# Performance work log

Hardware: AMD Instinct MI355X
Metric: run time of the kernel (lower is better)

Reference implementation:

```python
import jax, jax.numpy as jnp
import numpy as np

N, E, G = 100000, 1600000, 64
IN, H, OUT = 128, 64, 16  # hidden/2 = 32
SLOPE = 0.01


def setup_inputs() -> dict:
    key = jax.random.key(0)
    ks = jax.random.split(key, 7)
    features = jax.random.normal(ks[0], (N, IN), dtype=jnp.float32)
    src = jax.random.randint(ks[1], (E,), 0, N)
    dst = jax.random.randint(ks[2], (E,), 0, N)
    graph_ids = jnp.sort(jax.random.randint(ks[3], (N,), 0, G))
    # kaiming-uniform-ish fan_in init, bias=False everywhere
    W1 = jax.random.uniform(ks[4], (IN, H), jnp.float32, -1.0, 1.0) * np.sqrt(3.0 / IN)
    W2 = jax.random.uniform(ks[5], (H, H // 2), jnp.float32, -1.0, 1.0) * np.sqrt(3.0 / H)
    Wc = jax.random.uniform(ks[6], (H // 2, OUT), jnp.float32, -1.0, 1.0) * np.sqrt(3.0 / (H // 2))
    return {"features": features, "src": src, "dst": dst, "graph_ids": graph_ids,
            "W1": W1, "W2": W2, "Wc": Wc}


def _graph_conv(x, W, src, dst, n):
    # DGL GraphConv, norm='both', bias=False:
    # out = D_in^{-1/2} A (D_out^{-1/2} x) W   (degrees clamped to >= 1)
    ones = jnp.ones(src.shape[0], dtype=x.dtype)
    outdeg = jnp.clip(jax.ops.segment_sum(ones, src, num_segments=n), 1.0)
    indeg = jnp.clip(jax.ops.segment_sum(ones, dst, num_segments=n), 1.0)
    h = (x * jax.lax.rsqrt(outdeg)[:, None]) @ W  # project first (in_dim > out_dim)
    m = jax.ops.segment_sum(h[src], dst, num_segments=n)  # sparse aggregation
    return m * jax.lax.rsqrt(indeg)[:, None]


def reference(features, src, dst, graph_ids, W1, W2, Wc):
    h = jax.nn.leaky_relu(_graph_conv(features, W1, src, dst, N), SLOPE)
    h = jax.nn.leaky_relu(_graph_conv(h, W2, src, dst, N), SLOPE)
    # dropout is identity at inference
    sums = jax.ops.segment_sum(h, graph_ids, num_segments=G)
    cnts = jnp.clip(jax.ops.segment_sum(jnp.ones((N,), h.dtype), graph_ids, num_segments=G), 1.0)
    mean = sums / cnts[:, None]  # dgl.mean_nodes
    return mean @ Wc  # [G, OUT]
```

## Files before the change

### kernel.cpp

```cpp
#include <hip/hip_runtime.h>

#define NN 100000
#define NE 1600000
#define NG 64
#define D_IN 128
#define D_H 64
#define D_H2 32
#define D_OUT 16
#define SLOPE 0.01f
#define REC 48

#define BSH 9
#define NBK 196
#define NCB 250
#define CHE (NE / NCB)
#define PCAP 80

typedef _Float16 half2v __attribute__((ext_vector_type(2)));
typedef _Float16 h8 __attribute__((ext_vector_type(8)));
typedef float f32x4 __attribute__((ext_vector_type(4)));

__global__ __launch_bounds__(256) void p12_scatter(const int* __restrict__ src,
                                                   const int* __restrict__ dst,
                                                   unsigned* __restrict__ pkD,
                                                   unsigned short* __restrict__ pkS,
                                                   int* __restrict__ cntD,
                                                   int* __restrict__ cntS) {
  __shared__ int cD[NBK], cS[NBK];
  int b = blockIdx.x, t = threadIdx.x;
  for (int i = t; i < NBK; i += 256) { cD[i] = 0; cS[i] = 0; }
  __syncthreads();
  const int4* s4 = (const int4*)(src + b * CHE);
  const int4* d4 = (const int4*)(dst + b * CHE);
  for (int i = t; i < CHE / 4; i += 256) {
    int4 s = s4[i], d = d4[i];
#pragma unroll
    for (int j = 0; j < 4; ++j) {
      int ss = (j == 0) ? s.x : (j == 1) ? s.y : (j == 2) ? s.z : s.w;
      int dd = (j == 0) ? d.x : (j == 1) ? d.y : (j == 2) ? d.z : d.w;
      int kd = dd >> BSH;
      int pd = atomicAdd(&cD[kd], 1);
      if (pd < PCAP) pkD[((size_t)kd * NCB + b) * PCAP + pd] =
          ((unsigned)(dd & 511) << 17) | (unsigned)ss;
      int ks = ss >> BSH;
      int ps = atomicAdd(&cS[ks], 1);
      if (ps < PCAP) pkS[((size_t)ks * NCB + b) * PCAP + ps] =
          (unsigned short)(ss & 511);
    }
  }
  __syncthreads();
  for (int i = t; i < NBK; i += 256) {
    cntD[i * NCB + b] = min(cD[i], PCAP);
    cntS[i * NCB + b] = min(cS[i], PCAP);
  }
}

__global__ __launch_bounds__(256) void p3_build(const unsigned* __restrict__ pkD,
                                                const unsigned short* __restrict__ pkS,
                                                const int* __restrict__ cntD,
                                                const int* __restrict__ cntS,
                                                int* __restrict__ adj,
                                                int* __restrict__ indeg,
                                                int* __restrict__ outdeg) {
  __shared__ int hh[512];
  int bb = blockIdx.x, t = threadIdx.x;
  for (int i = t; i < 512; i += 256) hh[i] = 0;
  __syncthreads();
  if (bb < NBK) {
    int k = bb;
    int n0 = k << BSH;
    if (t < NCB) {
      int cnt = cntD[k * NCB + t];
      const uint4* r4 = (const uint4*)(pkD + ((size_t)k * NCB + t) * PCAP);
      for (int i = 0; i * 4 < cnt; ++i) {
        uint4 v = r4[i];
#pragma unroll
        for (int j = 0; j < 4; ++j) {
          int idx = i * 4 + j;
          if (idx < cnt) {
            unsigned rec = (j == 0) ? v.x : (j == 1) ? v.y : (j == 2) ? v.z : v.w;
            int local = rec >> 17;
            int pos = atomicAdd(&hh[local], 1);
            if (pos < REC) adj[(size_t)(n0 + local) * REC + pos] = (int)(rec & 0x1FFFF);
          }
        }
      }
    }
    __syncthreads();
    int4 ph = make_int4(NN, NN, NN, NN);
    for (int i = t; i < 512; i += 256) {
      int n = n0 + i;
      if (n < NN) {
        int dg = hh[i];
        indeg[n] = dg;
        int d = min(dg, REC);
        int dr = min((d + 15) & ~15, REC);
        int j = d;
        for (; j & 3; ++j) if (j < dr) adj[(size_t)n * REC + j] = NN;
        for (; j + 4 <= dr; j += 4) *(int4*)&adj[(size_t)n * REC + j] = ph;
      }
    }
  } else {
    int k = bb - NBK;
    if (t < NCB) {
      int cnt = cntS[k * NCB + t];
      const uint4* r4 = (const uint4*)(pkS + ((size_t)k * NCB + t) * PCAP);
      for (int i = 0; i * 8 < cnt; ++i) {
        uint4 v = r4[i];
        const unsigned short* u = (const unsigned short*)&v;
#pragma unroll
        for (int j = 0; j < 8; ++j) {
          int idx = i * 8 + j;
          if (idx < cnt) atomicAdd(&hh[u[j]], 1);
        }
      }
    }
    __syncthreads();
    int n0 = k << BSH;
    for (int i = t; i < 512; i += 256) {
      int n = n0 + i;
      if (n < NN) outdeg[n] = hh[i];
    }
  }
}

__global__ __launch_bounds__(256) void k_mm1f(const float* __restrict__ X,
                                              const float* __restrict__ W,
                                              const int* __restrict__ odeg,
                                              _Float16* __restrict__ Y) {
  __shared__ _Float16 Wt[64][136];
  int t = threadIdx.x;
  if (blockIdx.x == 0 && t < 64) Y[(size_t)NN * 64 + t] = (_Float16)0.f;
  for (int i = t; i < 128 * 64; i += 256) {
    int k = i >> 6, f = i & 63;
    Wt[f][k] = (_Float16)W[i];
  }
  __syncthreads();
  int lane = t & 63, w = t >> 6;
  int m = lane & 15, q = lane >> 4;
  h8 bf[4][4];
#pragma unroll
  for (int kc = 0; kc < 4; ++kc)
#pragma unroll
    for (int nt = 0; nt < 4; ++nt)
      bf[kc][nt] = *(const h8*)&Wt[nt * 16 + m][kc * 32 + q * 8];

  const int NT = NN / 16;
  int idx = blockIdx.x * 4 + w;
  int t0 = idx * 2, t1 = t0 + 1;
  f32x4 r0[8], r1[8];
  if (t0 < NT) {
    const f32x4* X0 = (const f32x4*)(X + (size_t)(t0 * 16 + m) * 128);
#pragma unroll
    for (int kc = 0; kc < 4; ++kc) {
      r0[kc * 2 + 0] = X0[kc * 8 + q * 2 + 0];
      r0[kc * 2 + 1] = X0[kc * 8 + q * 2 + 1];
    }
  }
  if (t1 < NT) {
    const f32x4* X1 = (const f32x4*)(X + (size_t)(t1 * 16 + m) * 128);
#pragma unroll
    for (int kc = 0; kc < 4; ++kc) {
      r1[kc * 2 + 0] = X1[kc * 8 + q * 2 + 0];
      r1[kc * 2 + 1] = X1[kc * 8 + q * 2 + 1];
    }
  }
#pragma unroll
  for (int half = 0; half < 2; ++half) {
    int tile = (half == 0) ? t0 : t1;
    if (tile >= NT) continue;
    f32x4* rr = (half == 0) ? r0 : r1;
    f32x4 acc[4] = {{0,0,0,0},{0,0,0,0},{0,0,0,0},{0,0,0,0}};
#pragma unroll
    for (int kc = 0; kc < 4; ++kc) {
      f32x4 x0 = rr[kc * 2 + 0], x1 = rr[kc * 2 + 1];
      h8 a;
      a[0] = (_Float16)x0.x; a[1] = (_Float16)x0.y;
      a[2] = (_Float16)x0.z; a[3] = (_Float16)x0.w;
      a[4] = (_Float16)x1.x; a[5] = (_Float16)x1.y;
      a[6] = (_Float16)x1.z; a[7] = (_Float16)x1.w;
#pragma unroll
      for (int nt = 0; nt < 4; ++nt)
        acc[nt] = __builtin_amdgcn_mfma_f32_16x16x32_f16(a, bf[kc][nt], acc[nt], 0, 0, 0);
    }
    int n0 = tile * 16;
#pragma unroll
    for (int reg = 0; reg < 4; ++reg) {
      int nn = n0 + q * 4 + reg;
      float sc = rsqrtf((float)max(odeg[nn], 1));
#pragma unroll
      for (int nt = 0; nt < 4; ++nt)
        Y[(size_t)nn * 64 + nt * 16 + m] = (_Float16)(acc[nt][reg] * sc);
    }
  }
}

__global__ __launch_bounds__(256) void k_aggmm2(const int* __restrict__ adj,
                                                const int* __restrict__ indeg,
                                                const int* __restrict__ odeg,
                                                const h8* __restrict__ H8,
                                                const float* __restrict__ W,
                                                _Float16* __restrict__ Y) {
  __shared__ _Float16 Ht[32][72];
  __shared__ _Float16 Wt[32][72];
  int t = threadIdx.x;
  if (blockIdx.x == 0 && t < 32) Y[(size_t)NN * 32 + t] = (_Float16)0.f;
  for (int i = t; i < 64 * 32; i += 256) {
    int k = i >> 5, f = i & 31;
    Wt[f][k] = (_Float16)W[i];
  }
  int l8 = t & 7;
  int nd = t >> 3;
  int node = blockIdx.x * 32 + nd;
  int deg = indeg[node];
  int groups = (min(deg, REC) + 15) >> 4;
  const int4* c4 = (const int4*)(adj + (size_t)node * REC);
  float acc[8] = {0.f, 0.f, 0.f, 0.f, 0.f, 0.f, 0.f, 0.f};
  for (int g = 0; g < groups; ++g) {
    int4 ca = c4[g * 4 + 0], cb = c4[g * 4 + 1];
    {
      h8 v0 = H8[(size_t)ca.x * 8 + l8];
      h8 v1 = H8[(size_t)ca.y * 8 + l8];
      h8 v2 = H8[(size_t)ca.z * 8 + l8];
      h8 v3 = H8[(size_t)ca.w * 8 + l8];
      h8 v4 = H8[(size_t)cb.x * 8 + l8];
      h8 v5 = H8[(size_t)cb.y * 8 + l8];
      h8 v6 = H8[(size_t)cb.z * 8 + l8];
      h8 v7 = H8[(size_t)cb.w * 8 + l8];
#pragma unroll
      for (int j = 0; j < 8; ++j)
        acc[j] += (((float)v0[j] + (float)v1[j]) + ((float)v2[j] + (float)v3[j])) +
                  (((float)v4[j] + (float)v5[j]) + ((float)v6[j] + (float)v7[j]));
    }
    int4 cc = c4[g * 4 + 2], cd = c4[g * 4 + 3];
    {
      h8 v0 = H8[(size_t)cc.x * 8 + l8];
      h8 v1 = H8[(size_t)cc.y * 8 + l8];
      h8 v2 = H8[(size_t)cc.z * 8 + l8];
      h8 v3 = H8[(size_t)cc.w * 8 + l8];
      h8 v4 = H8[(size_t)cd.x * 8 + l8];
      h8 v5 = H8[(size_t)cd.y * 8 + l8];
      h8 v6 = H8[(size_t)cd.z * 8 + l8];
      h8 v7 = H8[(size_t)cd.w * 8 + l8];
#pragma unroll
      for (int j = 0; j < 8; ++j)
        acc[j] += (((float)v0[j] + (float)v1[j]) + ((float)v2[j] + (float)v3[j])) +
                  (((float)v4[j] + (float)v5[j]) + ((float)v6[j] + (float)v7[j]));
    }
  }
  float sc = rsqrtf((float)max(deg, 1));
  h8 hv;
#pragma unroll
  for (int j = 0; j < 8; ++j) {
    float x = acc[j] * sc;
    hv[j] = (_Float16)((x > 0.f) ? x : SLOPE * x);
  }
  *(h8*)&Ht[nd][l8 * 8] = hv;
  __syncthreads();
  int lane = t & 63, w = t >> 6;
  if (w < 2) {
    int m = lane & 15, q = lane >> 4;
    h8 bf[2][2];
#pragma unroll
    for (int kc = 0; kc < 2; ++kc)
#pragma unroll
      for (int nt = 0; nt < 2; ++nt)
        bf[kc][nt] = *(const h8*)&Wt[nt * 16 + m][kc * 32 + q * 8];
    h8 af[2];
#pragma unroll
    for (int kc = 0; kc < 2; ++kc)
      af[kc] = *(const h8*)&Ht[w * 16 + m][kc * 32 + q * 8];
    f32x4 acc2[2] = {{0, 0, 0, 0}, {0, 0, 0, 0}};
#pragma unroll
    for (int kc = 0; kc < 2; ++kc)
#pragma unroll
      for (int nt = 0; nt < 2; ++nt)
        acc2[nt] = __builtin_amdgcn_mfma_f32_16x16x32_f16(af[kc], bf[kc][nt], acc2[nt], 0, 0, 0);
#pragma unroll
    for (int reg = 0; reg < 4; ++reg) {
      int nn = blockIdx.x * 32 + w * 16 + q * 4 + reg;
      float sco = rsqrtf((float)max(odeg[nn], 1));
#pragma unroll
      for (int nt = 0; nt < 2; ++nt)
        Y[(size_t)nn * 32 + nt * 16 + m] = (_Float16)(acc2[nt][reg] * sco);
    }
  }
}

__global__ __launch_bounds__(256) void k_agg32p(const int* __restrict__ adj,
                                                const int* __restrict__ indeg,
                                                const int* __restrict__ gid,
                                                const h8* __restrict__ H8,
                                                float* __restrict__ pool) {
  __shared__ float lp[4][D_H2];
  __shared__ int gmin_s;
  int t = threadIdx.x;
  int l4 = t & 3;
  int nd = t >> 2;
  int node = blockIdx.x * 64 + nd;
  bool valid = node < NN;
  int nclamp = valid ? node : NN - 1;
  if (t == 0) gmin_s = gid[blockIdx.x * 64];
  for (int i = t; i < 4 * D_H2; i += 256) ((float*)lp)[i] = 0.f;
  int deg = valid ? indeg[nclamp] : 0;
  int groups = (min(deg, REC) + 15) >> 4;
  const int4* c4 = (const int4*)(adj + (size_t)nclamp * REC);
  float acc[8] = {0.f, 0.f, 0.f, 0.f, 0.f, 0.f, 0.f, 0.f};
  for (int g = 0; g < groups; ++g) {
    int4 ca = c4[g * 4 + 0], cb = c4[g * 4 + 1];
    {
      h8 v0 = H8[(size_t)ca.x * 4 + l4];
      h8 v1 = H8[(size_t)ca.y * 4 + l4];
      h8 v2 = H8[(size_t)ca.z * 4 + l4];
      h8 v3 = H8[(size_t)ca.w * 4 + l4];
      h8 v4 = H8[(size_t)cb.x * 4 + l4];
      h8 v5 = H8[(size_t)cb.y * 4 + l4];
      h8 v6 = H8[(size_t)cb.z * 4 + l4];
      h8 v7 = H8[(size_t)cb.w * 4 + l4];
#pragma unroll
      for (int j = 0; j < 8; ++j)
        acc[j] += (((float)v0[j] + (float)v1[j]) + ((float)v2[j] + (float)v3[j])) +
                  (((float)v4[j] + (float)v5[j]) + ((float)v6[j] + (float)v7[j]));
    }
    int4 cc = c4[g * 4 + 2], cd = c4[g * 4 + 3];
    {
      h8 v0 = H8[(size_t)cc.x * 4 + l4];
      h8 v1 = H8[(size_t)cc.y * 4 + l4];
      h8 v2 = H8[(size_t)cc.z * 4 + l4];
      h8 v3 = H8[(size_t)cc.w * 4 + l4];
      h8 v4 = H8[(size_t)cd.x * 4 + l4];
      h8 v5 = H8[(size_t)cd.y * 4 + l4];
      h8 v6 = H8[(size_t)cd.z * 4 + l4];
      h8 v7 = H8[(size_t)cd.w * 4 + l4];
#pragma unroll
      for (int j = 0; j < 8; ++j)
        acc[j] += (((float)v0[j] + (float)v1[j]) + ((float)v2[j] + (float)v3[j])) +
                  (((float)v4[j] + (float)v5[j]) + ((float)v6[j] + (float)v7[j]));
    }
  }
  __syncthreads();
  if (valid) {
    float sc = rsqrtf((float)max(deg, 1));
    int gl = min(gid[node] - gmin_s, 3);
#pragma unroll
    for (int j = 0; j < 8; ++j) {
      float x = acc[j] * sc;
      x = (x > 0.f) ? x : SLOPE * x;
      atomicAdd(&lp[gl][l4 * 8 + j], x);
    }
  }
  __syncthreads();
  if (t < 4 * D_H2) {
    float v = ((float*)lp)[t];
    if (v != 0.f) {
      int gl = t >> 5, f = t & 31;
      atomicAdd(&pool[(gmin_s + gl) * D_H2 + f], v);
    }
  }
}

__global__ __launch_bounds__(256) void k_out(const float* __restrict__ pool,
                                             const int* __restrict__ gid,
                                             const float* __restrict__ Wc,
                                             float* __restrict__ out) {
  __shared__ int bnd[NG + 1];
  __shared__ float mean[NG][D_H2];
  int t = threadIdx.x;
  if (t <= NG) {
    int target = t;
    int lo = 0, hi = NN;
    while (lo < hi) {
      int mid = (lo + hi) >> 1;
      if (gid[mid] < target) lo = mid + 1; else hi = mid;
    }
    bnd[t] = lo;
  }
  __syncthreads();
  for (int i = t; i < NG * D_H2; i += 256) {
    int g = i >> 5;
    float inv = 1.0f / (float)max(bnd[g + 1] - bnd[g], 1);
    ((float*)mean)[i] = pool[i] * inv;
  }
  __syncthreads();
  for (int i = t; i < NG * D_OUT; i += 256) {
    int g = i / D_OUT, o = i % D_OUT;
    float s = 0.f;
#pragma unroll
    for (int c = 0; c < D_H2; ++c) s += mean[g][c] * Wc[c * D_OUT + o];
    out[i] = s;
  }
}

extern "C" void kernel_launch(void* const* d_in, const int* in_sizes, int n_in,
                              void* d_out, int out_size, void* d_ws, size_t ws_size,
                              hipStream_t stream) {
  const float* X  = (const float*)d_in[0];
  const int*   src = (const int*)d_in[1];
  const int*   dst = (const int*)d_in[2];
  const int*   gid = (const int*)d_in[3];
  const float* W1 = (const float*)d_in[4];
  const float* W2 = (const float*)d_in[5];
  const float* Wc = (const float*)d_in[6];
  float* out = (float*)d_out;

  char* p = (char*)d_ws;
  auto alloc = [&](size_t bytes) {
    char* q = p;
    p += (bytes + 255) & ~(size_t)255;
    return q;
  };
  float*          pool   = (float*)alloc(NG * D_H2 * 4);
  int*            outdeg = (int*)alloc(NN * 4);
  int*            indeg  = (int*)alloc(NN * 4);
  int*            cntD   = (int*)alloc((size_t)NBK * NCB * 4);
  int*            cntS   = (int*)alloc((size_t)NBK * NCB * 4);
  unsigned*       pkD    = (unsigned*)alloc((size_t)NBK * NCB * PCAP * 4);
  unsigned short* pkS    = (unsigned short*)alloc((size_t)NBK * NCB * PCAP * 2);
  int*            adj    = (int*)alloc((size_t)NN * REC * 4);
  _Float16*       bufA   = (_Float16*)alloc((size_t)(NN + 1) * 64 * 2);
  _Float16*       bufC   = (_Float16*)alloc((size_t)(NN + 1) * 32 * 2);

  hipMemsetAsync(pool, 0, NG * D_H2 * 4, stream);

  p12_scatter<<<NCB, 256, 0, stream>>>(src, dst, pkD, pkS, cntD, cntS);
  p3_build<<<2 * NBK, 256, 0, stream>>>(pkD, pkS, cntD, cntS, adj, indeg, outdeg);

  k_mm1f<<<782, 256, 0, stream>>>(X, W1, outdeg, bufA);
  k_aggmm2<<<NN / 32, 256, 0, stream>>>(adj, indeg, outdeg, (const h8*)bufA, W2, bufC);
  k_agg32p<<<(NN + 63) / 64, 256, 0, stream>>>(adj, indeg, gid, (const h8*)bufC, pool);
  k_out<<<1, 256, 0, stream>>>(pool, gid, Wc, out);
}
```

Baseline: 219.2 us.

## Stage adjacency rows in LDS and pad neighbor lists to 8 instead of 16

The aggregation kernels now copy each block's adjacency rows and degrees into shared memory with coalesced int4 loads, then read neighbor indices from LDS. Neighbor lists are padded to a multiple of 8 rather than 16, so fewer dummy gathers of the padding node are issued. The edge-partition count doubles to 500 with a smaller per-bucket cap, and the build kernel loops over buckets to match. The costs are extra LDS use per block, an added barrier, and a higher chance of bucket overflow under the smaller cap.

```diff
diff --git a/kernel.cpp b/kernel.cpp
--- a/kernel.cpp
+++ b/kernel.cpp
@@ -12,9 +12,9 @@
 
 #define BSH 9
 #define NBK 196
-#define NCB 250
+#define NCB 500
 #define CHE (NE / NCB)
-#define PCAP 80
+#define PCAP 56
 
 typedef _Float16 half2v __attribute__((ext_vector_type(2)));
 typedef _Float16 h8 __attribute__((ext_vector_type(8)));
@@ -69,9 +69,9 @@
   if (bb < NBK) {
     int k = bb;
     int n0 = k << BSH;
-    if (t < NCB) {
-      int cnt = cntD[k * NCB + t];
-      const uint4* r4 = (const uint4*)(pkD + ((size_t)k * NCB + t) * PCAP);
+    for (int s = t; s < NCB; s += 256) {
+      int cnt = cntD[k * NCB + s];
+      const uint4* r4 = (const uint4*)(pkD + ((size_t)k * NCB + s) * PCAP);
       for (int i = 0; i * 4 < cnt; ++i) {
         uint4 v = r4[i];
 #pragma unroll
@@ -94,7 +94,7 @@
         int dg = hh[i];
         indeg[n] = dg;
         int d = min(dg, REC);
-        int dr = min((d + 15) & ~15, REC);
+        int dr = min((d + 7) & ~7, REC);
         int j = d;
         for (; j & 3; ++j) if (j < dr) adj[(size_t)n * REC + j] = NN;
         for (; j + 4 <= dr; j += 4) *(int4*)&adj[(size_t)n * REC + j] = ph;
@@ -102,9 +102,9 @@
     }
   } else {
     int k = bb - NBK;
-    if (t < NCB) {
-      int cnt = cntS[k * NCB + t];
-      const uint4* r4 = (const uint4*)(pkS + ((size_t)k * NCB + t) * PCAP);
+    for (int s = t; s < NCB; s += 256) {
+      int cnt = cntS[k * NCB + s];
+      const uint4* r4 = (const uint4*)(pkS + ((size_t)k * NCB + s) * PCAP);
       for (int i = 0; i * 8 < cnt; ++i) {
         uint4 v = r4[i];
         const unsigned short* u = (const unsigned short*)&v;
@@ -201,6 +201,8 @@
                                                 const h8* __restrict__ H8,
                                                 const float* __restrict__ W,
                                                 _Float16* __restrict__ Y) {
+  __shared__ int Adj[32][REC];
+  __shared__ int Deg[32];
   __shared__ _Float16 Ht[32][72];
   __shared__ _Float16 Wt[32][72];
   int t = threadIdx.x;
@@ -209,44 +211,34 @@
     int k = i >> 5, f = i & 31;
     Wt[f][k] = (_Float16)W[i];
   }
+  int node0 = blockIdx.x * 32;
+  {
+    const int4* gadj = (const int4*)(adj + (size_t)node0 * REC);
+    for (int i = t; i < 32 * (REC / 4); i += 256)
+      ((int4*)Adj)[i] = gadj[i];
+    if (t < 32) Deg[t] = indeg[node0 + t];
+  }
+  __syncthreads();
   int l8 = t & 7;
   int nd = t >> 3;
-  int node = blockIdx.x * 32 + nd;
-  int deg = indeg[node];
-  int groups = (min(deg, REC) + 15) >> 4;
-  const int4* c4 = (const int4*)(adj + (size_t)node * REC);
+  int deg = Deg[nd];
+  int groups = (min(deg, REC) + 7) >> 3;
   float acc[8] = {0.f, 0.f, 0.f, 0.f, 0.f, 0.f, 0.f, 0.f};
   for (int g = 0; g < groups; ++g) {
-    int4 ca = c4[g * 4 + 0], cb = c4[g * 4 + 1];
-    {
-      h8 v0 = H8[(size_t)ca.x * 8 + l8];
-      h8 v1 = H8[(size_t)ca.y * 8 + l8];
-      h8 v2 = H8[(size_t)ca.z * 8 + l8];
-      h8 v3 = H8[(size_t)ca.w * 8 + l8];
-      h8 v4 = H8[(size_t)cb.x * 8 + l8];
-      h8 v5 = H8[(size_t)cb.y * 8 + l8];
-      h8 v6 = H8[(size_t)cb.z * 8 + l8];
-      h8 v7 = H8[(size_t)cb.w * 8 + l8];
-#pragma unroll
-      for (int j = 0; j < 8; ++j)
-        acc[j] += (((float)v0[j] + (float)v1[j]) + ((float)v2[j] + (float)v3[j])) +
-                  (((float)v4[j] + (float)v5[j]) + ((float)v6[j] + (float)v7[j]));
-    }
-    int4 cc = c4[g * 4 + 2], cd = c4[g * 4 + 3];
-    {
-      h8 v0 = H8[(size_t)cc.x * 8 + l8];
-      h8 v1 = H8[(size_t)cc.y * 8 + l8];
-      h8 v2 = H8[(size_t)cc.z * 8 + l8];
-      h8 v3 = H8[(size_t)cc.w * 8 + l8];
-      h8 v4 = H8[(size_t)cd.x * 8 + l8];
-      h8 v5 = H8[(size_t)cd.y * 8 + l8];
-      h8 v6 = H8[(size_t)cd.z * 8 + l8];
-      h8 v7 = H8[(size_t)cd.w * 8 + l8];
-#pragma unroll
-      for (int j = 0; j < 8; ++j)
-        acc[j] += (((float)v0[j] + (float)v1[j]) + ((float)v2[j] + (float)v3[j])) +
-                  (((float)v4[j] + (float)v5[j]) + ((float)v6[j] + (float)v7[j]));
-    }
+    int4 ca = *(const int4*)&Adj[nd][g * 8 + 0];
+    int4 cb = *(const int4*)&Adj[nd][g * 8 + 4];
+    h8 v0 = H8[(size_t)ca.x * 8 + l8];
+    h8 v1 = H8[(size_t)ca.y * 8 + l8];
+    h8 v2 = H8[(size_t)ca.z * 8 + l8];
+    h8 v3 = H8[(size_t)ca.w * 8 + l8];
+    h8 v4 = H8[(size_t)cb.x * 8 + l8];
+    h8 v5 = H8[(size_t)cb.y * 8 + l8];
+    h8 v6 = H8[(size_t)cb.z * 8 + l8];
+    h8 v7 = H8[(size_t)cb.w * 8 + l8];
+#pragma unroll
+    for (int j = 0; j < 8; ++j)
+      acc[j] += (((float)v0[j] + (float)v1[j]) + ((float)v2[j] + (float)v3[j])) +
+                (((float)v4[j] + (float)v5[j]) + ((float)v6[j] + (float)v7[j]));
   }
   float sc = rsqrtf((float)max(deg, 1));
   h8 hv;
@@ -292,53 +284,45 @@
                                                 const int* __restrict__ gid,
                                                 const h8* __restrict__ H8,
                                                 float* __restrict__ pool) {
+  __shared__ int Adj2[64][REC];
+  __shared__ int Deg2[64];
   __shared__ float lp[4][D_H2];
   __shared__ int gmin_s;
   int t = threadIdx.x;
   int l4 = t & 3;
   int nd = t >> 2;
-  int node = blockIdx.x * 64 + nd;
+  int node0 = blockIdx.x * 64;
+  int node = node0 + nd;
   bool valid = node < NN;
-  int nclamp = valid ? node : NN - 1;
-  if (t == 0) gmin_s = gid[blockIdx.x * 64];
+  if (t == 0) gmin_s = gid[node0];
   for (int i = t; i < 4 * D_H2; i += 256) ((float*)lp)[i] = 0.f;
-  int deg = valid ? indeg[nclamp] : 0;
-  int groups = (min(deg, REC) + 15) >> 4;
-  const int4* c4 = (const int4*)(adj + (size_t)nclamp * REC);
+  {
+    int maxi = (min(NN - node0, 64)) * (REC / 4);
+    const int4* gadj = (const int4*)(adj + (size_t)node0 * REC);
+    for (int i = t; i < 64 * (REC / 4); i += 256)
+      ((int4*)Adj2)[i] = (i < maxi) ? gadj[i] : make_int4(NN, NN, NN, NN);
+    if (t < 64) Deg2[t] = (node0 + t < NN) ? indeg[node0 + t] : 0;
+  }
+  __syncthreads();
+  int deg = Deg2[nd];
+  int groups = (min(deg, REC) + 7) >> 3;
   float acc[8] = {0.f, 0.f, 0.f, 0.f, 0.f, 0.f, 0.f, 0.f};
   for (int g = 0; g < groups; ++g) {
-    int4 ca = c4[g * 4 + 0], cb = c4[g * 4 + 1];
-    {
-      h8 v0 = H8[(size_t)ca.x * 4 + l4];
-      h8 v1 = H8[(size_t)ca.y * 4 + l4];
-      h8 v2 = H8[(size_t)ca.z * 4 + l4];
-      h8 v3 = H8[(size_t)ca.w * 4 + l4];
-      h8 v4 = H8[(size_t)cb.x * 4 + l4];
-      h8 v5 = H8[(size_t)cb.y * 4 + l4];
-      h8 v6 = H8[(size_t)cb.z * 4 + l4];
-      h8 v7 = H8[(size_t)cb.w * 4 + l4];
-#pragma unroll
-      for (int j = 0; j < 8; ++j)
-        acc[j] += (((float)v0[j] + (float)v1[j]) + ((float)v2[j] + (float)v3[j])) +
-                  (((float)v4[j] + (float)v5[j]) + ((float)v6[j] + (float)v7[j]));
-    }
-    int4 cc = c4[g * 4 + 2], cd = c4[g * 4 + 3];
-    {
-      h8 v0 = H8[(size_t)cc.x * 4 + l4];
-      h8 v1 = H8[(size_t)cc.y * 4 + l4];
-      h8 v2 = H8[(size_t)cc.z * 4 + l4];
-      h8 v3 = H8[(size_t)cc.w * 4 + l4];
-      h8 v4 = H8[(size_t)cd.x * 4 + l4];
-      h8 v5 = H8[(size_t)cd.y * 4 + l4];
-      h8 v6 = H8[(size_t)cd.z * 4 + l4];
-      h8 v7 = H8[(size_t)cd.w * 4 + l4];
-#pragma unroll
-      for (int j = 0; j < 8; ++j)
-        acc[j] += (((float)v0[j] + (float)v1[j]) + ((float)v2[j] + (float)v3[j])) +
-                  (((float)v4[j] + (float)v5[j]) + ((float)v6[j] + (float)v7[j]));
-    }
-  }
-  __syncthreads();
+    int4 ca = *(const int4*)&Adj2[nd][g * 8 + 0];
+    int4 cb = *(const int4*)&Adj2[nd][g * 8 + 4];
+    h8 v0 = H8[(size_t)ca.x * 4 + l4];
+    h8 v1 = H8[(size_t)ca.y * 4 + l4];
+    h8 v2 = H8[(size_t)ca.z * 4 + l4];
+    h8 v3 = H8[(size_t)ca.w * 4 + l4];
+    h8 v4 = H8[(size_t)cb.x * 4 + l4];
+    h8 v5 = H8[(size_t)cb.y * 4 + l4];
+    h8 v6 = H8[(size_t)cb.z * 4 + l4];
+    h8 v7 = H8[(size_t)cb.w * 4 + l4];
+#pragma unroll
+    for (int j = 0; j < 8; ++j)
+      acc[j] += (((float)v0[j] + (float)v1[j]) + ((float)v2[j] + (float)v3[j])) +
+                (((float)v4[j] + (float)v5[j]) + ((float)v6[j] + (float)v7[j]));
+  }
   if (valid) {
     float sc = rsqrtf((float)max(deg, 1));
     int gl = min(gid[node] - gmin_s, 3);
```

Result: no change. 218.4 us (-0.4%).
